# Performance work log

Hardware: AMD Instinct MI355X
Metric: run time of the kernel (lower is better)

## Reference

```python
import jax, jax.numpy as jnp
import numpy as np

N_NODES = 100000
N_EDGES = 3200000
D_IN = 128
D_OUT = 128


def setup_inputs() -> dict:
    key = jax.random.key(0)
    k1, k2, k3, k4 = jax.random.split(key, 4)
    features = jax.random.normal(k1, (N_NODES, D_IN), dtype=jnp.float32)
    src = jax.random.randint(k2, (N_EDGES,), 0, N_NODES, dtype=jnp.int32)
    dst = jax.random.randint(k3, (N_EDGES,), 0, N_NODES, dtype=jnp.int32)
    # nn.Linear params (Kaiming-uniform-ish init scale)
    bound = 1.0 / np.sqrt(D_IN)
    W = jax.random.uniform(k4, (D_IN, D_OUT), dtype=jnp.float32, minval=-bound, maxval=bound)
    b = jnp.zeros((D_OUT,), dtype=jnp.float32)
    return {"features": features, "W": W, "b": b, "src": src, "dst": dst}


def reference(features, W, b, src, dst):
    # message: gather source node features per edge  [E, D_IN]
    msg = features[src]
    # mean_reduce: segment mean over in-edges per destination node
    summed = jax.ops.segment_sum(msg, dst, num_segments=N_NODES)
    deg = jax.ops.segment_sum(jnp.ones((msg.shape[0],), dtype=features.dtype), dst, num_segments=N_NODES)
    deg = deg[:, None]
    # DGL semantics: nodes with no incoming messages keep their original 'h'
    h = jnp.where(deg > 0, summed / jnp.maximum(deg, 1.0), features)
    # node_update: linear + activation applied to all nodes
    return jax.nn.relu(h @ W + b)
```

## Files before the change

kernel.cpp:

```cpp
#include <hip/hip_runtime.h>

#define N_NODES 100000
#define N_EDGES 3200000
#define D 128

#define BSHIFT 6
#define BNODES 64
#define NBUCK  1563
#define CAP    2432
#define PART_TILE 8192
#define PART_THREADS 512
#define NB_PART ((N_EDGES + PART_TILE - 1) / PART_TILE)
#define CPL 25

#define OFF_GCUR  0
#define OFF_PART  2048
#define FEATB_OFF 15213056ULL
#define WPK_OFF   40813056ULL

typedef __attribute__((ext_vector_type(8))) short short8_t;
typedef __attribute__((ext_vector_type(4))) float f32x4;

__device__ __forceinline__ ushort f2bf(float x) {
    unsigned u = __float_as_uint(x);
    unsigned r = u + 0x7FFFu + ((u >> 16) & 1u);
    return (ushort)(r >> 16);
}
__device__ __forceinline__ float blo(unsigned v) { return __uint_as_float(v << 16); }
__device__ __forceinline__ float bhi(unsigned v) { return __uint_as_float(v & 0xFFFF0000u); }

__global__ __launch_bounds__(256) void gcn_cvt_kernel(
    const float* __restrict__ in, ushort* __restrict__ out, int n8)
{
    int i = blockIdx.x * 256 + threadIdx.x;
    if (i >= n8) return;
    const float4* p = (const float4*)in + (size_t)i * 2;
    float4 a = p[0], b = p[1];
    ushort4 r0 = make_ushort4(f2bf(a.x), f2bf(a.y), f2bf(a.z), f2bf(a.w));
    ushort4 r1 = make_ushort4(f2bf(b.x), f2bf(b.y), f2bf(b.z), f2bf(b.w));
    ushort4* q = (ushort4*)out + (size_t)i * 2;
    q[0] = r0;
    q[1] = r1;
}

__global__ __launch_bounds__(256) void gcn_wpack_kernel(
    const float* __restrict__ W, ushort* __restrict__ wpk)
{
    int tid = blockIdx.x * 256 + threadIdx.x;
    if (tid >= 32 * 64) return;
    int f = tid >> 6, l = tid & 63;
    int n4 = f >> 2, k4 = f & 3;
    int col = n4 * 16 + (l & 15);
    int kb  = k4 * 32 + ((l >> 4) << 3);
    ushort* q = wpk + (size_t)tid * 8;
    #pragma unroll
    for (int t = 0; t < 8; ++t) q[t] = f2bf(W[(kb + t) * D + col]);
}

__global__ void gcn_init_kernel(int* __restrict__ gcur)
{
    int t = blockIdx.x * 256 + threadIdx.x;
    if (t < NBUCK) gcur[t] = t * CAP;
}

__global__ __launch_bounds__(PART_THREADS) void gcn_part_kernel(
    const int* __restrict__ src, const int* __restrict__ dst,
    int* __restrict__ gcur, int* __restrict__ part)
{
    __shared__ int cnt[NBUCK];
    __shared__ int lbase[NBUCK + 1];
    __shared__ int gbase[NBUCK];
    __shared__ int stage[PART_TILE];
    __shared__ ushort sbuck[PART_TILE];

    int t = threadIdx.x;
    int eb = blockIdx.x * PART_TILE;
    int nT = N_EDGES - eb; if (nT > PART_TILE) nT = PART_TILE;

    for (int i = t; i < NBUCK; i += PART_THREADS) cnt[i] = 0;
    __syncthreads();

    #pragma unroll
    for (int it = 0; it < PART_TILE / PART_THREADS; ++it) {
        int e = it * PART_THREADS + t;
        if (e < nT) atomicAdd(&cnt[dst[eb + e] >> BSHIFT], 1);
    }
    __syncthreads();

    if (t < 64) {
        int v[CPL];
        int s = 0;
        #pragma unroll
        for (int j = 0; j < CPL; ++j) {
            int i = t * CPL + j;
            v[j] = (i < NBUCK) ? cnt[i] : 0;
            s += v[j];
        }
        int inc = s;
        #pragma unroll
        for (int d = 1; d < 64; d <<= 1) {
            int up = __shfl_up(inc, d, 64);
            if (t >= d) inc += up;
        }
        int run = inc - s;
        #pragma unroll
        for (int j = 0; j < CPL; ++j) {
            int i = t * CPL + j;
            if (i < NBUCK) lbase[i] = run;
            run += v[j];
        }
        if (t == 63) lbase[NBUCK] = run;
    }
    __syncthreads();

    for (int i = t; i < NBUCK; i += PART_THREADS) {
        int c = lbase[i + 1] - lbase[i];
        gbase[i] = c ? atomicAdd(&gcur[i], c) : 0;
        cnt[i] = 0;
    }
    __syncthreads();

    #pragma unroll
    for (int it = 0; it < PART_TILE / PART_THREADS; ++it) {
        int e = it * PART_THREADS + t;
        if (e < nT) {
            int dvv = dst[eb + e];
            int svv = src[eb + e];
            int b  = dvv >> BSHIFT;
            int dl = dvv & (BNODES - 1);
            int pos = lbase[b] + atomicAdd(&cnt[b], 1);
            stage[pos] = (dl << 17) | svv;
            sbuck[pos] = (ushort)b;
        }
    }
    __syncthreads();

    for (int i = t; i < nT; i += PART_THREADS) {
        int b = sbuck[i];
        part[gbase[b] + (i - lbase[b])] = stage[i];
    }
}

__global__ __launch_bounds__(256) void gcn_fused_kernel(
    const float* __restrict__ feat,
    const ushort* __restrict__ featb,
    const ushort* __restrict__ wpk,
    const float* __restrict__ bias,
    const int* __restrict__ gcur,
    const int* __restrict__ part,
    float* __restrict__ out)
{
    __shared__ int stage[CAP];
    __shared__ int stage2[CAP];
    __shared__ int ldeg[BNODES];
    __shared__ int loff[BNODES];
    __shared__ int lcur[BNODES];
    __shared__ ushort hlds[16 * 136];

    int t = threadIdx.x, lane = t & 63, w = t >> 6;
    int k = blockIdx.x;

    short8_t wb[8];
    #pragma unroll
    for (int j = 0; j < 8; ++j)
        wb[j] = *(const short8_t*)(wpk + ((size_t)(w * 8 + j) * 64 + lane) * 8);
    float bj[2];
    bj[0] = bias[(2 * w) * 16 + (lane & 15)];
    bj[1] = bias[(2 * w + 1) * 16 + (lane & 15)];

    int pb = k * CAP;
    int nE = gcur[k] - pb;
    if (nE > CAP) nE = CAP;

    if (t < BNODES) ldeg[t] = 0;
    __syncthreads();

    for (int i = t; i < nE; i += 256) {
        int pk = part[pb + i];
        stage[i] = pk;
        atomicAdd(&ldeg[pk >> 17], 1);
    }
    __syncthreads();

    if (t < 64) {
        int v = ldeg[t];
        int inc = v;
        #pragma unroll
        for (int d = 1; d < 64; d <<= 1) {
            int up = __shfl_up(inc, d, 64);
            if (t >= d) inc += up;
        }
        loff[t] = inc - v;
        lcur[t] = inc - v;
    }
    __syncthreads();

    for (int i = t; i < nE; i += 256) {
        int pk = stage[i];
        int p = atomicAdd(&lcur[pk >> 17], 1);
        stage2[p] = pk & 0x1FFFF;
    }

    #pragma unroll 1
    for (int si = 0; si < 4; ++si) {
        __syncthreads();

        #pragma unroll
        for (int i = 0; i < 4; ++i) {
            int nl = si * 16 + w * 4 + i;
            int r  = k * BNODES + nl;
            float s0 = 0.0f, s1 = 0.0f;
            if (r < N_NODES) {
                int dg = ldeg[nl], beg = loff[nl];
                if (dg == 0) {
                    float2 f2 = *(const float2*)(feat + (size_t)r * D + lane * 2);
                    s0 = f2.x; s1 = f2.y;
                } else {
                    int p = beg, e = beg + dg;
                    for (; p + 8 <= e; p += 8) {
                        int i0 = stage2[p],     i1 = stage2[p + 1], i2 = stage2[p + 2], i3 = stage2[p + 3];
                        int i4 = stage2[p + 4], i5 = stage2[p + 5], i6 = stage2[p + 6], i7 = stage2[p + 7];
                        unsigned v0 = *(const unsigned*)(featb + ((size_t)i0 << 7) + lane * 2);
                        unsigned v1 = *(const unsigned*)(featb + ((size_t)i1 << 7) + lane * 2);
                        unsigned v2 = *(const unsigned*)(featb + ((size_t)i2 << 7) + lane * 2);
                        unsigned v3 = *(const unsigned*)(featb + ((size_t)i3 << 7) + lane * 2);
                        unsigned v4 = *(const unsigned*)(featb + ((size_t)i4 << 7) + lane * 2);
                        unsigned v5 = *(const unsigned*)(featb + ((size_t)i5 << 7) + lane * 2);
                        unsigned v6 = *(const unsigned*)(featb + ((size_t)i6 << 7) + lane * 2);
                        unsigned v7 = *(const unsigned*)(featb + ((size_t)i7 << 7) + lane * 2);
                        s0 += blo(v0) + blo(v1) + blo(v2) + blo(v3);
                        s1 += bhi(v0) + bhi(v1) + bhi(v2) + bhi(v3);
                        s0 += blo(v4) + blo(v5) + blo(v6) + blo(v7);
                        s1 += bhi(v4) + bhi(v5) + bhi(v6) + bhi(v7);
                    }
                    for (; p + 4 <= e; p += 4) {
                        int i0 = stage2[p], i1 = stage2[p + 1], i2 = stage2[p + 2], i3 = stage2[p + 3];
                        unsigned v0 = *(const unsigned*)(featb + ((size_t)i0 << 7) + lane * 2);
                        unsigned v1 = *(const unsigned*)(featb + ((size_t)i1 << 7) + lane * 2);
                        unsigned v2 = *(const unsigned*)(featb + ((size_t)i2 << 7) + lane * 2);
                        unsigned v3 = *(const unsigned*)(featb + ((size_t)i3 << 7) + lane * 2);
                        s0 += blo(v0) + blo(v1) + blo(v2) + blo(v3);
                        s1 += bhi(v0) + bhi(v1) + bhi(v2) + bhi(v3);
                    }
                    for (; p < e; ++p) {
                        unsigned v = *(const unsigned*)(featb + ((size_t)stage2[p] << 7) + lane * 2);
                        s0 += blo(v); s1 += bhi(v);
                    }
                    float inv = 1.0f / (float)dg;
                    s0 *= inv; s1 *= inv;
                }
            }
            unsigned pk = ((unsigned)f2bf(s1) << 16) | (unsigned)f2bf(s0);
            *(unsigned*)(&hlds[(w * 4 + i) * 136 + lane * 2]) = pk;
        }
        __syncthreads();

        short8_t a[4];
        #pragma unroll
        for (int k4 = 0; k4 < 4; ++k4)
            a[k4] = *(const short8_t*)(&hlds[(lane & 15) * 136 + k4 * 32 + ((lane >> 4) << 3)]);

        int rowb = k * BNODES + si * 16 + ((lane >> 4) << 2);
        #pragma unroll
        for (int nt = 0; nt < 2; ++nt) {
            f32x4 acc = { bj[nt], bj[nt], bj[nt], bj[nt] };
            #pragma unroll
            for (int k4 = 0; k4 < 4; ++k4)
                acc = __builtin_amdgcn_mfma_f32_16x16x32_bf16(a[k4], wb[nt * 4 + k4], acc, 0, 0, 0);
            int col = (2 * w + nt) * 16 + (lane & 15);
            #pragma unroll
            for (int rr = 0; rr < 4; ++rr)
                if (rowb + rr < N_NODES)
                    out[(size_t)(rowb + rr) * D + col] = fmaxf(acc[rr], 0.0f);
        }
    }
}

extern "C" void kernel_launch(void* const* d_in, const int* in_sizes, int n_in,
                              void* d_out, int out_size, void* d_ws, size_t ws_size,
                              hipStream_t stream) {
    const float* feat = (const float*)d_in[0];
    const float* W    = (const float*)d_in[1];
    const float* bias = (const float*)d_in[2];
    const int*   src  = (const int*)d_in[3];
    const int*   dst  = (const int*)d_in[4];
    float* out = (float*)d_out;

    int* ib   = (int*)d_ws;
    int* gcur = ib + OFF_GCUR;
    int* part = ib + OFF_PART;
    ushort* featb = (ushort*)((char*)d_ws + FEATB_OFF);
    ushort* wpk   = (ushort*)((char*)d_ws + WPK_OFF);

    {
        int n8 = N_NODES * D / 8;
        gcn_cvt_kernel<<<(n8 + 255) / 256, 256, 0, stream>>>(feat, featb, n8);
    }
    gcn_wpack_kernel<<<8, 256, 0, stream>>>(W, wpk);
    gcn_init_kernel<<<(NBUCK + 255) / 256, 256, 0, stream>>>(gcur);
    gcn_part_kernel<<<NB_PART, PART_THREADS, 0, stream>>>(src, dst, gcur, part);
    gcn_fused_kernel<<<NBUCK, 256, 0, stream>>>(feat, featb, wpk, bias, gcur, part, out);
}
```

Before: 289.9 us.

## Split edge bucketing into two-level radix partition by destination

Replaces the single-pass partition into 1563 fine buckets with two passes: first into 98 coarse buckets of 1024 nodes, then each coarse bucket is split into 16 fine bins of 64 nodes. The aim is to cut the many scattered, poorly coalesced global writes and the heavy per-block atomics and scan over 1563 buckets. In exchange it adds an extra kernel and a full extra read and write of the edge list, and it uses fixed capacities that silently drop edges if a bucket overflows.

```diff
diff --git a/kernel.cpp b/kernel.cpp
--- a/kernel.cpp
+++ b/kernel.cpp
@@ -4,19 +4,21 @@
 #define N_EDGES 3200000
 #define D 128
 
-#define BSHIFT 6
+#define NC1    98
+#define CAP1   33792
+#define NCHUNK 5
+#define NB1    391
+#define FB     1568
+#define CAP2   2432
+#define NBUCK  1563
 #define BNODES 64
-#define NBUCK  1563
-#define CAP    2432
-#define PART_TILE 8192
-#define PART_THREADS 512
-#define NB_PART ((N_EDGES + PART_TILE - 1) / PART_TILE)
-#define CPL 25
-
-#define OFF_GCUR  0
-#define OFF_PART  2048
-#define FEATB_OFF 15213056ULL
-#define WPK_OFF   40813056ULL
+
+#define OFF_GCUR1 0
+#define OFF_GCUR2 128
+#define OFF_PART1 2048
+#define OFF_PART2 3313664
+#define FEATB_OFF 28508160ULL
+#define WPK_OFF   54108160ULL
 
 typedef __attribute__((ext_vector_type(8))) short short8_t;
 typedef __attribute__((ext_vector_type(4))) float f32x4;
@@ -57,87 +59,152 @@
     for (int t = 0; t < 8; ++t) q[t] = f2bf(W[(kb + t) * D + col]);
 }
 
-__global__ void gcn_init_kernel(int* __restrict__ gcur)
-{
-    int t = blockIdx.x * 256 + threadIdx.x;
-    if (t < NBUCK) gcur[t] = t * CAP;
-}
-
-__global__ __launch_bounds__(PART_THREADS) void gcn_part_kernel(
+__global__ __launch_bounds__(512) void gcn_part1_kernel(
     const int* __restrict__ src, const int* __restrict__ dst,
-    int* __restrict__ gcur, int* __restrict__ part)
-{
-    __shared__ int cnt[NBUCK];
-    __shared__ int lbase[NBUCK + 1];
-    __shared__ int gbase[NBUCK];
-    __shared__ int stage[PART_TILE];
-    __shared__ ushort sbuck[PART_TILE];
+    int* __restrict__ gcur1, int* __restrict__ part1)
+{
+    __shared__ int cnt[NC1];
+    __shared__ int lbase[NC1 + 1];
+    __shared__ int gbase[NC1];
+    __shared__ int stage[8192];
+    __shared__ unsigned char sb[8192];
 
     int t = threadIdx.x;
-    int eb = blockIdx.x * PART_TILE;
-    int nT = N_EDGES - eb; if (nT > PART_TILE) nT = PART_TILE;
-
-    for (int i = t; i < NBUCK; i += PART_THREADS) cnt[i] = 0;
-    __syncthreads();
-
-    #pragma unroll
-    for (int it = 0; it < PART_TILE / PART_THREADS; ++it) {
-        int e = it * PART_THREADS + t;
-        if (e < nT) atomicAdd(&cnt[dst[eb + e] >> BSHIFT], 1);
+    int eb = blockIdx.x * 8192;
+    int nT = N_EDGES - eb; if (nT > 8192) nT = 8192;
+
+    for (int i = t; i < NC1; i += 512) cnt[i] = 0;
+    __syncthreads();
+
+    int dv[16], sv[16];
+    #pragma unroll
+    for (int it = 0; it < 16; ++it) {
+        int e = eb + it * 512 + t;
+        bool ok = e < N_EDGES;
+        dv[it] = ok ? dst[e] : -1;
+        sv[it] = ok ? src[e] : 0;
+        if (ok) atomicAdd(&cnt[dv[it] >> 10], 1);
     }
     __syncthreads();
 
     if (t < 64) {
-        int v[CPL];
-        int s = 0;
-        #pragma unroll
-        for (int j = 0; j < CPL; ++j) {
-            int i = t * CPL + j;
-            v[j] = (i < NBUCK) ? cnt[i] : 0;
-            s += v[j];
-        }
-        int inc = s;
+        int i0 = 2 * t, i1 = 2 * t + 1;
+        int v0 = (i0 < NC1) ? cnt[i0] : 0;
+        int v1 = (i1 < NC1) ? cnt[i1] : 0;
+        int p = v0 + v1, inc = p;
         #pragma unroll
         for (int d = 1; d < 64; d <<= 1) {
             int up = __shfl_up(inc, d, 64);
             if (t >= d) inc += up;
         }
-        int run = inc - s;
-        #pragma unroll
-        for (int j = 0; j < CPL; ++j) {
-            int i = t * CPL + j;
-            if (i < NBUCK) lbase[i] = run;
-            run += v[j];
-        }
-        if (t == 63) lbase[NBUCK] = run;
-    }
-    __syncthreads();
-
-    for (int i = t; i < NBUCK; i += PART_THREADS) {
+        int ex = inc - p;
+        if (i0 < NC1) lbase[i0] = ex;
+        if (i1 < NC1) lbase[i1] = ex + v0;
+        if (t == 63) lbase[NC1] = inc;
+    }
+    __syncthreads();
+
+    for (int i = t; i < NC1; i += 512) {
         int c = lbase[i + 1] - lbase[i];
-        gbase[i] = c ? atomicAdd(&gcur[i], c) : 0;
+        gbase[i] = c ? atomicAdd(&gcur1[i], c) : 0;
         cnt[i] = 0;
     }
     __syncthreads();
 
     #pragma unroll
-    for (int it = 0; it < PART_TILE / PART_THREADS; ++it) {
-        int e = it * PART_THREADS + t;
-        if (e < nT) {
-            int dvv = dst[eb + e];
-            int svv = src[eb + e];
-            int b  = dvv >> BSHIFT;
-            int dl = dvv & (BNODES - 1);
+    for (int it = 0; it < 16; ++it) {
+        if (dv[it] >= 0) {
+            int b  = dv[it] >> 10;
+            int dl = dv[it] & 1023;
             int pos = lbase[b] + atomicAdd(&cnt[b], 1);
-            stage[pos] = (dl << 17) | svv;
-            sbuck[pos] = (ushort)b;
-        }
-    }
-    __syncthreads();
-
-    for (int i = t; i < nT; i += PART_THREADS) {
-        int b = sbuck[i];
-        part[gbase[b] + (i - lbase[b])] = stage[i];
+            stage[pos] = (dl << 17) | sv[it];
+            sb[pos] = (unsigned char)b;
+        }
+    }
+    __syncthreads();
+
+    for (int i = t; i < nT; i += 512) {
+        int b = sb[i];
+        int slot = gbase[b] + (i - lbase[b]);
+        if (slot < CAP1) part1[(size_t)b * CAP1 + slot] = stage[i];
+    }
+}
+
+__global__ __launch_bounds__(512) void gcn_part2_kernel(
+    const int* __restrict__ gcur1, const int* __restrict__ part1,
+    int* __restrict__ gcur2, int* __restrict__ part2)
+{
+    __shared__ int hist[8][17];
+    __shared__ int wcur[8][17];
+    __shared__ int lbase[17];
+    __shared__ int gbase[16];
+    __shared__ int stage[8192];
+    __shared__ unsigned char sbin[8192];
+
+    int t = threadIdx.x, w = t >> 6;
+    int c = blockIdx.x / NCHUNK;
+    int chunk = blockIdx.x % NCHUNK;
+
+    int cn = gcur1[c]; if (cn > CAP1) cn = CAP1;
+    int beg = chunk * 8192;
+    int nT = cn - beg;
+    if (nT <= 0) return;
+    if (nT > 8192) nT = 8192;
+
+    if (t < 16) {
+        #pragma unroll
+        for (int ww = 0; ww < 8; ++ww) hist[ww][t] = 0;
+    }
+    __syncthreads();
+
+    const int* p1 = part1 + (size_t)c * CAP1 + beg;
+
+    #pragma unroll
+    for (int it = 0; it < 16; ++it) {
+        int i = it * 512 + t;
+        if (i < nT) atomicAdd(&hist[w][p1[i] >> 23], 1);
+    }
+    __syncthreads();
+
+    if (t < 16) {
+        int tot = 0;
+        #pragma unroll
+        for (int ww = 0; ww < 8; ++ww) {
+            int x = hist[ww][t];
+            hist[ww][t] = tot;
+            tot += x;
+        }
+        int inc = tot;
+        #pragma unroll
+        for (int d = 1; d < 16; d <<= 1) {
+            int up = __shfl_up(inc, d, 64);
+            if (t >= d) inc += up;
+        }
+        int ex = inc - tot;
+        lbase[t] = ex;
+        gbase[t] = tot ? atomicAdd(&gcur2[c * 16 + t], tot) : 0;
+        #pragma unroll
+        for (int ww = 0; ww < 8; ++ww) wcur[ww][t] = ex + hist[ww][t];
+    }
+    __syncthreads();
+
+    #pragma unroll
+    for (int it = 0; it < 16; ++it) {
+        int i = it * 512 + t;
+        if (i < nT) {
+            int word = p1[i];
+            int f = word >> 23;
+            int pos = atomicAdd(&wcur[w][f], 1);
+            stage[pos] = word & 0x7FFFFF;
+            sbin[pos] = (unsigned char)f;
+        }
+    }
+    __syncthreads();
+
+    for (int i = t; i < nT; i += 512) {
+        int f = sbin[i];
+        int slot = gbase[f] + (i - lbase[f]);
+        if (slot < CAP2) part2[((size_t)c * 16 + f) * CAP2 + slot] = stage[i];
     }
 }
 
@@ -146,12 +213,12 @@
     const ushort* __restrict__ featb,
     const ushort* __restrict__ wpk,
     const float* __restrict__ bias,
-    const int* __restrict__ gcur,
+    const int* __restrict__ gcnt,
     const int* __restrict__ part,
     float* __restrict__ out)
 {
-    __shared__ int stage[CAP];
-    __shared__ int stage2[CAP];
+    __shared__ int stage[CAP2];
+    __shared__ int stage2[CAP2];
     __shared__ int ldeg[BNODES];
     __shared__ int loff[BNODES];
     __shared__ int lcur[BNODES];
@@ -168,9 +235,9 @@
     bj[0] = bias[(2 * w) * 16 + (lane & 15)];
     bj[1] = bias[(2 * w + 1) * 16 + (lane & 15)];
 
-    int pb = k * CAP;
-    int nE = gcur[k] - pb;
-    if (nE > CAP) nE = CAP;
+    size_t pb = (size_t)k * CAP2;
+    int nE = gcnt[k];
+    if (nE > CAP2) nE = CAP2;
 
     if (t < BNODES) ldeg[t] = 0;
     __syncthreads();
@@ -286,18 +353,22 @@
     const int*   dst  = (const int*)d_in[4];
     float* out = (float*)d_out;
 
-    int* ib   = (int*)d_ws;
-    int* gcur = ib + OFF_GCUR;
-    int* part = ib + OFF_PART;
+    int* ib    = (int*)d_ws;
+    int* gcur1 = ib + OFF_GCUR1;
+    int* gcur2 = ib + OFF_GCUR2;
+    int* part1 = ib + OFF_PART1;
+    int* part2 = ib + OFF_PART2;
     ushort* featb = (ushort*)((char*)d_ws + FEATB_OFF);
     ushort* wpk   = (ushort*)((char*)d_ws + WPK_OFF);
+
+    hipMemsetAsync(ib, 0, 2048 * sizeof(int), stream);
 
     {
         int n8 = N_NODES * D / 8;
         gcn_cvt_kernel<<<(n8 + 255) / 256, 256, 0, stream>>>(feat, featb, n8);
     }
     gcn_wpack_kernel<<<8, 256, 0, stream>>>(W, wpk);
-    gcn_init_kernel<<<(NBUCK + 255) / 256, 256, 0, stream>>>(gcur);
-    gcn_part_kernel<<<NB_PART, PART_THREADS, 0, stream>>>(src, dst, gcur, part);
-    gcn_fused_kernel<<<NBUCK, 256, 0, stream>>>(feat, featb, wpk, bias, gcur, part, out);
-}
+    gcn_part1_kernel<<<NB1, 512, 0, stream>>>(src, dst, gcur1, part1);
+    gcn_part2_kernel<<<NC1 * NCHUNK, 512, 0, stream>>>(gcur1, part1, gcur2, part2);
+    gcn_fused_kernel<<<NBUCK, 256, 0, stream>>>(feat, featb, wpk, bias, gcur2, part2, out);
+}
```

Result: no change. 289.8 us (-0.0%).
